# Optimization experiments

Measured on AMD Instinct MI355X. Metric: run time of the kernel, lower is better.

## Reference

```python
import jax, jax.numpy as jnp
import numpy as np

B, S, IN_DIM, EMBED, HEADS, WINDOW = 2, 2048, 1024, 1024, 16, 256
HEAD_DIM = EMBED // HEADS
NEG_FILL = -9.0e15


def setup_inputs() -> dict:
    key = jax.random.key(0)
    k1, k2, k3, k4 = jax.random.split(key, 4)
    x = jax.random.normal(k1, (B, S, IN_DIM), dtype=jnp.float32)
    # padding_mask: positions with value 1 get zeroed in q/k/v (matches masked_fill semantics)
    padding_mask = jax.random.randint(k2, (B, S), 0, 2, dtype=jnp.int32)
    # xavier-uniform-like init scale for the linear weights
    lim_qkv = np.sqrt(6.0 / (IN_DIM + 3 * EMBED)).astype(np.float32)
    lim_o = np.sqrt(6.0 / (EMBED + EMBED)).astype(np.float32)
    Wqkv = jax.random.uniform(k3, (3 * EMBED, IN_DIM), jnp.float32, -lim_qkv, lim_qkv)
    bqkv = jnp.zeros((3 * EMBED,), jnp.float32)
    Wo = jax.random.uniform(k4, (EMBED, EMBED), jnp.float32, -lim_o, lim_o)
    bo = jnp.zeros((EMBED,), jnp.float32)
    return {"x": x, "padding_mask": padding_mask, "Wqkv": Wqkv, "bqkv": bqkv, "Wo": Wo, "bo": bo}


def reference(x, padding_mask, Wqkv, bqkv, Wo, bo):
    b, s, _ = x.shape
    h, hd, pad = HEADS, HEAD_DIM, WINDOW // 2
    # qkv projection: torch Linear is x @ W.T + b
    qkv = x @ Wqkv.T + bqkv                      # [B, S, 3E]
    qkv = qkv.reshape(b, s, h, 3 * hd).transpose(0, 2, 1, 3)  # [B, H, S, 3*hd]
    q, k, v = jnp.split(qkv, 3, axis=-1)          # each [B, H, S, hd]
    # zero out padded positions in q, k, v where padding_mask == 1
    pm = (padding_mask != 0)[:, None, :, None]    # [B, 1, S, 1]
    q = jnp.where(pm, 0.0, q)
    k = jnp.where(pm, 0.0, k)
    v = jnp.where(pm, 0.0, v)
    # dense banded scores: identical math to the unfold-based band compute
    scores = jnp.einsum("bhsd,bhtd->bhst", q, k)  # [B, H, S, S]
    idx = jnp.arange(s)
    band = jnp.abs(idx[None, :] - idx[:, None]) <= pad  # |i-j| <= window/2
    scores = jnp.where(band, scores, jnp.float32(NEG_FILL))
    scores = scores / jnp.sqrt(jnp.float32(hd))   # original scales AFTER the fill
    attn = jax.nn.softmax(scores, axis=-1)        # [B, H, S, S]
    vals = jnp.einsum("bhst,bhtd->bhsd", attn, v)  # [B, H, S, hd]
    vals = vals.transpose(0, 2, 1, 3).reshape(b, s, h * hd)  # [B, S, E]
    return vals @ Wo.T + bo
```

## Files before the change

kernel.cpp:

```cpp
#include <hip/hip_runtime.h>
#include <stdint.h>

#define S_LEN 2048
#define EMBED 1024
#define HEADS 16
#define HD 64
#define M_ROWS 4096
#define N_QKV 3072
#define KDIM 1024
#define SP 2336
#define CLP2 200

typedef __attribute__((ext_vector_type(8))) short short8;
typedef __attribute__((ext_vector_type(4))) float f32x4;

__device__ __forceinline__ unsigned short f2bf(float f) {
  union { float f; uint32_t u; } c; c.f = f;
  uint32_t u = c.u;
  u += 0x7fffu + ((u >> 16) & 1u);
  return (unsigned short)(u >> 16);
}

__device__ __forceinline__ void gload_lds16(const unsigned short* g, unsigned short* l) {
  __builtin_amdgcn_global_load_lds(
      (const __attribute__((address_space(1))) void*)g,
      (__attribute__((address_space(3))) void*)l, 16, 0, 0);
}

#define XQ 1048576
#define WQKVQ 786432
#define WOQ 262144
#define CVTQ (XQ + WQKVQ + WOQ)
__global__ __launch_bounds__(256) void cvt3_kernel(
    const float* __restrict__ x, const float* __restrict__ wqkv, const float* __restrict__ wo,
    unsigned short* __restrict__ xb, unsigned short* __restrict__ wqkvb, unsigned short* __restrict__ wob,
    unsigned short* __restrict__ vTp) {
  int i = blockIdx.x * blockDim.x + threadIdx.x;
  if (i < CVTQ) {
    const float* s; unsigned short* d; int off;
    if (i < XQ)               { s = x;    d = xb;    off = i; }
    else if (i < XQ + WQKVQ)  { s = wqkv; d = wqkvb; off = i - XQ; }
    else                      { s = wo;   d = wob;   off = i - XQ - WQKVQ; }
    float4 f = reinterpret_cast<const float4*>(s)[off];
    ushort4 o;
    o.x = f2bf(f.x); o.y = f2bf(f.y); o.z = f2bf(f.z); o.w = f2bf(f.w);
    reinterpret_cast<ushort4*>(d)[off] = o;
  } else {
    int j = i - CVTQ;
    int row = j / 72, p = j % 72;
    int off = row * 584 + (p < 32 ? p : 544 + (p - 32));
    reinterpret_cast<ushort4*>(vTp)[off] = (ushort4){0, 0, 0, 0};
  }
}

__global__ __launch_bounds__(512, 2) void gemm_qkv(
    const unsigned short* __restrict__ A, const unsigned short* __restrict__ Bm,
    const float* __restrict__ bias, const int* __restrict__ pm,
    unsigned short* __restrict__ qo, unsigned short* __restrict__ ko,
    unsigned short* __restrict__ vTp)
{
  __shared__ __align__(16) unsigned short smem[57344];
  const int t = threadIdx.x, wave = t >> 6, lane = t & 63;
  const int m16 = lane & 15, q4 = lane >> 4;
  const int wm = wave >> 1, wn = wave & 1;
  const int bid = blockIdx.x;
  const int mb = bid >> 4, nb = bid & 15;
  const int lrow = lane >> 3;
  const int lsegsw = ((lane & 7) ^ lrow) * 8;
  const unsigned short* gsrc[7];
#pragma unroll
  for (int j = 0; j < 7; j++) {
    int u = wave * 7 + j;
    gsrc[j] = (u < 32 ? A  + (size_t)(mb * 256 + u * 8 + lrow) * KDIM
                      : Bm + (size_t)(nb * 192 + (u - 32) * 8 + lrow) * KDIM)
              + lsegsw;
  }
  const int rsw = (m16 & 7) * 8;

  f32x4 acc[4][6];
#pragma unroll
  for (int i_ = 0; i_ < 4; i_++)
#pragma unroll
    for (int j_ = 0; j_ < 6; j_++) acc[i_][j_] = (f32x4){0.f, 0.f, 0.f, 0.f};

  auto LDA = [&](short8* af, const unsigned short* As, int h) {
#pragma unroll
    for (int mt = 0; mt < 4; mt++)
      af[mt] = *reinterpret_cast<const short8*>(
          &As[(wm * 64 + mt * 16 + m16) * 64 + (((h * 4 + q4) * 8) ^ rsw)]);
  };
  auto LDB3 = [&](short8* bf, const unsigned short* Bs, int h, int n0) {
#pragma unroll
    for (int nt = 0; nt < 3; nt++)
      bf[nt] = *reinterpret_cast<const short8*>(
          &Bs[(wn * 96 + (n0 + nt) * 16 + m16) * 64 + (((h * 4 + q4) * 8) ^ rsw)]);
  };
  auto MM3 = [&](short8* af, short8* bf, int n0) {
#pragma unroll
    for (int mt = 0; mt < 4; mt++)
#pragma unroll
      for (int nt = 0; nt < 3; nt++)
        acc[mt][n0 + nt] =
            __builtin_amdgcn_mfma_f32_16x16x32_bf16(af[mt], bf[nt], acc[mt][n0 + nt], 0, 0, 0);
  };

#pragma unroll
  for (int j = 0; j < 7; j++)
    gload_lds16(gsrc[j], smem + (wave * 7 + j) * 512);
  __builtin_amdgcn_sched_barrier(0);

  for (int T = 0; T < 16; ++T) {
    const int c = T & 1;
    const unsigned short* As = smem + c * 28672;
    const unsigned short* Bs = As + 16384;
    unsigned short* nslab = smem + (c ^ 1) * 28672;
    const int nkt = (T + 1) * 64;
    const bool st = (T < 15);
    short8 af[4], bf[3];

    if (st) {
#pragma unroll
      for (int j = 0; j < 3; j++)
        gload_lds16(gsrc[j] + nkt, nslab + (wave * 7 + j) * 512);
    }
    __builtin_amdgcn_sched_barrier(0);
    if (st) asm volatile("s_waitcnt vmcnt(3)" ::: "memory");
    else    asm volatile("s_waitcnt vmcnt(0)" ::: "memory");
    __builtin_amdgcn_sched_barrier(0);
    __builtin_amdgcn_s_barrier();
    __builtin_amdgcn_sched_barrier(0);
    LDA(af, As, 0);
    LDB3(bf, Bs, 0, 0);
    asm volatile("s_waitcnt lgkmcnt(0)" ::: "memory");
    __builtin_amdgcn_sched_barrier(0);
    __builtin_amdgcn_s_setprio(1);
    MM3(af, bf, 0);
    __builtin_amdgcn_s_setprio(0);
    __builtin_amdgcn_sched_barrier(0);
    __builtin_amdgcn_s_barrier();
    __builtin_amdgcn_sched_barrier(0);

    LDB3(bf, Bs, 0, 3);
    if (st) {
#pragma unroll
      for (int j = 3; j < 5; j++)
        gload_lds16(gsrc[j] + nkt, nslab + (wave * 7 + j) * 512);
    }
    __builtin_amdgcn_sched_barrier(0);
    __builtin_amdgcn_s_barrier();
    asm volatile("s_waitcnt lgkmcnt(0)" ::: "memory");
    __builtin_amdgcn_sched_barrier(0);
    __builtin_amdgcn_s_setprio(1);
    MM3(af, bf, 3);
    __builtin_amdgcn_s_setprio(0);
    __builtin_amdgcn_sched_barrier(0);
    __builtin_amdgcn_s_barrier();
    __builtin_amdgcn_sched_barrier(0);

    LDA(af, As, 1);
    LDB3(bf, Bs, 1, 0);
    if (st) {
#pragma unroll
      for (int j = 5; j < 7; j++)
        gload_lds16(gsrc[j] + nkt, nslab + (wave * 7 + j) * 512);
    }
    __builtin_amdgcn_sched_barrier(0);
    __builtin_amdgcn_s_barrier();
    asm volatile("s_waitcnt lgkmcnt(0)" ::: "memory");
    __builtin_amdgcn_sched_barrier(0);
    __builtin_amdgcn_s_setprio(1);
    MM3(af, bf, 0);
    __builtin_amdgcn_s_setprio(0);
    __builtin_amdgcn_sched_barrier(0);
    __builtin_amdgcn_s_barrier();
    __builtin_amdgcn_sched_barrier(0);

    LDB3(bf, Bs, 1, 3);
    __builtin_amdgcn_sched_barrier(0);
    __builtin_amdgcn_s_barrier();
    asm volatile("s_waitcnt lgkmcnt(0)" ::: "memory");
    __builtin_amdgcn_sched_barrier(0);
    __builtin_amdgcn_s_setprio(1);
    MM3(af, bf, 3);
    __builtin_amdgcn_s_setprio(0);
    __builtin_amdgcn_sched_barrier(0);
    __builtin_amdgcn_s_barrier();
    __builtin_amdgcn_sched_barrier(0);
  }

  float pmv[4][4];
#pragma unroll
  for (int mt = 0; mt < 4; mt++)
#pragma unroll
    for (int reg = 0; reg < 4; reg++) {
      int row = mb * 256 + wm * 64 + mt * 16 + q4 * 4 + reg;
      pmv[mt][reg] = (pm[row] != 0) ? 0.0f : 1.0f;
    }
#pragma unroll
  for (int nt = 0; nt < 6; nt++) {
    int cloc = wn * 96 + nt * 16 + m16;
    float bv = bias[nb * 192 + cloc];
#pragma unroll
    for (int mt = 0; mt < 4; mt++) {
#pragma unroll
      for (int reg = 0; reg < 4; reg++) {
        int rloc = wm * 64 + mt * 16 + q4 * 4 + reg;
        smem[rloc * CLP2 + cloc] = f2bf((acc[mt][nt][reg] + bv) * pmv[mt][reg]);
      }
    }
  }
  __syncthreads();
  const int s0 = mb * 256;
  const int bh = (s0 >> 11) * 16 + nb, s0l = s0 & 2047;
  {
    int r = t >> 1, half = t & 1;
    const unsigned short* sq = &smem[r * CLP2 + half * 32];
    unsigned short* dq = qo + ((size_t)(bh * 2048 + s0l + r)) * 64 + half * 32;
#pragma unroll
    for (int j = 0; j < 4; j++)
      *reinterpret_cast<short8*>(dq + j * 8) = *reinterpret_cast<const short8*>(sq + j * 8);
    const unsigned short* sk = &smem[r * CLP2 + 64 + half * 32];
    unsigned short* dk = ko + ((size_t)(bh * 2048 + s0l + r)) * 64 + half * 32;
#pragma unroll
    for (int j = 0; j < 4; j++)
      *reinterpret_cast<short8*>(dk + j * 8) = *reinterpret_cast<const short8*>(sk + j * 8);
  }
  {
    int d = t & 63, oct = t >> 6;
    unsigned short* dst = vTp + (size_t)(bh * 64 + d) * SP + 128 + s0l + oct * 32;
#pragma unroll
    for (int j8 = 0; j8 < 4; j8++) {
      short8 tmp;
#pragma unroll
      for (int jj = 0; jj < 8; jj++)
        tmp[jj] = (short)smem[(oct * 32 + j8 * 8 + jj) * CLP2 + 128 + d];
      *reinterpret_cast<short8*>(dst + j8 * 8) = tmp;
    }
  }
}

__global__ __launch_bounds__(256) void gemm_out(
    const unsigned short* __restrict__ A, const unsigned short* __restrict__ Bm,
    const float* __restrict__ bias, float* __restrict__ out)
{
  __shared__ __align__(16) unsigned char smemraw[49152];
  float* Cldf = (float*)smemraw;
  const int t = threadIdx.x, wave = t >> 6, lane = t & 63;
  const int m16 = lane & 15, q4 = lane >> 4;
  const int wm = wave >> 1, wn = wave & 1;
  const int flat = blockIdx.y * 8 + blockIdx.x;
  const int xcd = flat & 7, bi = flat >> 3;
  const int mb = xcd * 8 + (bi & 7);
  const int nb = bi >> 3;
  const int srow = lane >> 2, scol = (lane & 3) << 3;
  const unsigned short* pA  = A + (size_t)(mb * 64 + wave * 16 + srow) * KDIM + scol;
  const unsigned short* pB0 = Bm + (size_t)(nb * 128 + wave * 32 + srow) * KDIM + scol;
  const unsigned short* pB1 = pB0 + 16 * KDIM;
  f32x4 acc[2][4];
#pragma unroll
  for (int i_ = 0; i_ < 2; i_++)
#pragma unroll
    for (int j_ = 0; j_ < 4; j_++) acc[i_][j_] = (f32x4){0.f, 0.f, 0.f, 0.f};

  auto stage = [&](int buf, int kt) {
    unsigned short* As = (unsigned short*)smemraw + buf * 12288;
    unsigned short* Bs = As + 4096;
#pragma unroll
    for (int h = 0; h < 2; h++) {
      gload_lds16(pA + kt + h * 32,  As + h * 2048 + (wave * 16) * 32);
      gload_lds16(pB0 + kt + h * 32, Bs + h * 4096 + (wave * 32) * 32);
      gload_lds16(pB1 + kt + h * 32, Bs + h * 4096 + (wave * 32 + 16) * 32);
    }
  };

  stage(0, 0);
  __builtin_amdgcn_sched_barrier(0);
  int cur = 0;
  for (int kt = 0; kt < KDIM; kt += 64) {
    const bool st = (kt + 64 < KDIM);
    if (st) stage(cur ^ 1, kt + 64);
    __builtin_amdgcn_sched_barrier(0);
    if (st) asm volatile("s_waitcnt vmcnt(6)" ::: "memory");
    else    asm volatile("s_waitcnt vmcnt(0)" ::: "memory");
    __builtin_amdgcn_sched_barrier(0);
    __builtin_amdgcn_s_barrier();
    __builtin_amdgcn_sched_barrier(0);
    const unsigned short* As = (const unsigned short*)smemraw + cur * 12288;
    const unsigned short* Bs = As + 4096;
#pragma unroll
    for (int h = 0; h < 2; h++) {
      short8 af[2], bf[4];
#pragma unroll
      for (int mt = 0; mt < 2; mt++)
        af[mt] = *reinterpret_cast<const short8*>(&As[h * 2048 + (wm * 32 + mt * 16 + m16) * 32 + q4 * 8]);
#pragma unroll
      for (int nt = 0; nt < 4; nt++)
        bf[nt] = *reinterpret_cast<const short8*>(&Bs[h * 4096 + (wn * 64 + nt * 16 + m16) * 32 + q4 * 8]);
#pragma unroll
      for (int mt = 0; mt < 2; mt++)
#pragma unroll
        for (int nt = 0; nt < 4; nt++)
          acc[mt][nt] = __builtin_amdgcn_mfma_f32_16x16x32_bf16(af[mt], bf[nt], acc[mt][nt], 0, 0, 0);
    }
    __builtin_amdgcn_sched_barrier(0);
    __builtin_amdgcn_s_barrier();
    __builtin_amdgcn_sched_barrier(0);
    cur ^= 1;
  }

#pragma unroll
  for (int nt = 0; nt < 4; nt++) {
    int cloc = wn * 64 + nt * 16 + m16;
    float bv = bias[nb * 128 + cloc];
#pragma unroll
    for (int mt = 0; mt < 2; mt++) {
#pragma unroll
      for (int reg = 0; reg < 4; reg++) {
        int rloc = wm * 32 + mt * 16 + q4 * 4 + reg;
        Cldf[rloc * 132 + cloc] = acc[mt][nt][reg] + bv;
      }
    }
  }
  __syncthreads();
  {
    int r = t >> 2, seg = t & 3;
    float* dst = out + (size_t)(mb * 64 + r) * EMBED + nb * 128 + seg * 32;
    const float* srcl = &Cldf[r * 132 + seg * 32];
#pragma unroll
    for (int j = 0; j < 8; j++)
      *reinterpret_cast<float4*>(dst + j * 4) = *reinterpret_cast<const float4*>(srcl + j * 4);
  }
}

__global__ __launch_bounds__(256, 2) void attn_kernel(
    const unsigned short* __restrict__ q, const unsigned short* __restrict__ k,
    const unsigned short* __restrict__ vTp, unsigned short* __restrict__ vals)
{
  __shared__ __align__(16) unsigned short smem[40960];
  unsigned short* Ks = smem;
  unsigned short* Vs = smem + 20480;
  unsigned short* Pld = smem;

  const int bid = blockIdx.x;
  const int bh = bid & 31, qg = bid >> 5;
  const int lane = threadIdx.x & 63, wave = threadIdx.x >> 6;
  const int i0b = qg * 64;
  const int i0 = i0b + wave * 16;
  const int m16 = lane & 15, q4 = lane >> 4;

  const unsigned short* qb = q + ((size_t)(bh * 2048 + i0 + m16)) * 64 + q4 * 8;
  short8 aq0 = *reinterpret_cast<const short8*>(qb);
  short8 aq1 = *reinterpret_cast<const short8*>(qb + 32);
  __builtin_amdgcn_sched_barrier(0);

  const unsigned short* kbase = k + (size_t)bh * 2048 * 64;
#pragma unroll
  for (int n = 0; n < 10; n++) {
    int idx = (n * 4 + wave) * 64 + lane;
    int krow = idx >> 3, seg = idx & 7;
    int grow = i0b - 128 + krow;
    grow = grow < 0 ? 0 : (grow > 2047 ? 2047 : grow);
    int lseg = seg ^ (krow & 7);
    gload_lds16(kbase + (size_t)grow * 64 + lseg * 8, Ks + (n * 4 + wave) * 512);
  }
  __builtin_amdgcn_sched_barrier(0);
  const unsigned short* vbase = vTp + (size_t)bh * 64 * SP + i0b;
#pragma unroll
  for (int n = 0; n < 10; n++) {
    int idx = (n * 4 + wave) * 64 + lane;
    int vrow = idx / 40, rem = idx % 40;
    int l = (rem & ~7) | ((rem & 7) ^ (vrow & 7));
    gload_lds16(vbase + (size_t)vrow * SP + l * 8, Vs + (n * 4 + wave) * 512);
  }
  __builtin_amdgcn_sched_barrier(0);

  asm volatile("s_waitcnt vmcnt(10)" ::: "memory");
  __builtin_amdgcn_sched_barrier(0);
  __builtin_amdgcn_s_barrier();
  __builtin_amdgcn_sched_barrier(0);

  float sum[4] = {0.f, 0.f, 0.f, 0.f};
  uint32_t pP[18][2];
#pragma unroll
  for (int ct = 0; ct < 18; ct++) {
    int r = (wave + ct) * 16 + m16;
    int js = i0b - 128 + r;
    const unsigned short* kr = Ks + r * 64;
    short8 b0 = *reinterpret_cast<const short8*>(kr + ((q4 ^ (r & 7)) * 8));
    short8 b1 = *reinterpret_cast<const short8*>(kr + (((q4 + 4) ^ (r & 7)) * 8));
    f32x4 a = {0.f, 0.f, 0.f, 0.f};
    a = __builtin_amdgcn_mfma_f32_16x16x32_bf16(aq0, b0, a, 0, 0, 0);
    a = __builtin_amdgcn_mfma_f32_16x16x32_bf16(aq1, b1, a, 0, 0, 0);
    unsigned short pe[4];
#pragma unroll
    for (int reg = 0; reg < 4; reg++) {
      int i = i0 + q4 * 4 + reg;
      bool valid = (js >= 0) && (js < 2048) && (js >= i - 128) && (js <= i + 128);
      float e = valid ? __expf(a[reg] * 0.125f) : 0.0f;
      sum[reg] += e;
      pe[reg] = f2bf(e);
    }
    pP[ct][0] = (uint32_t)pe[0] | ((uint32_t)pe[1] << 16);
    pP[ct][1] = (uint32_t)pe[2] | ((uint32_t)pe[3] << 16);
  }
  float rden[4];
#pragma unroll
  for (int reg = 0; reg < 4; reg++) {
    float s = sum[reg];
    s += __shfl_xor(s, 1);
    s += __shfl_xor(s, 2);
    s += __shfl_xor(s, 4);
    s += __shfl_xor(s, 8);
    rden[reg] = 1.0f / s;
  }

  __syncthreads();

  unsigned short* Pw = Pld + wave * 16 * 296;
#pragma unroll
  for (int ct = 0; ct < 18; ct++) {
    Pw[(q4 * 4 + 0) * 296 + ct * 16 + m16] = (unsigned short)(pP[ct][0] & 0xFFFF);
    Pw[(q4 * 4 + 1) * 296 + ct * 16 + m16] = (unsigned short)(pP[ct][0] >> 16);
    Pw[(q4 * 4 + 2) * 296 + ct * 16 + m16] = (unsigned short)(pP[ct][1] & 0xFFFF);
    Pw[(q4 * 4 + 3) * 296 + ct * 16 + m16] = (unsigned short)(pP[ct][1] >> 16);
  }
  short8 ap[9];
#pragma unroll
  for (int kc = 0; kc < 9; kc++)
    ap[kc] = *reinterpret_cast<const short8*>(&Pw[m16 * 296 + kc * 32 + q4 * 8]);

  const int b = bh >> 4, h = bh & 15;
#pragma unroll
  for (int dt = 0; dt < 4; dt++) {
    int vrow = dt * 16 + m16;
    const unsigned short* vr = Vs + vrow * 320;
    f32x4 av = {0.f, 0.f, 0.f, 0.f};
#pragma unroll
    for (int kc = 0; kc < 9; kc++) {
      int jseg = kc * 4 + wave * 2 + q4;
      if (jseg > 39) jseg = 39;
      int sseg = (jseg & ~7) | ((jseg & 7) ^ (vrow & 7));
      short8 bv = *reinterpret_cast<const short8*>(vr + sseg * 8);
      av = __builtin_amdgcn_mfma_f32_16x16x32_bf16(ap[kc], bv, av, 0, 0, 0);
    }
#pragma unroll
    for (int reg = 0; reg < 4; reg++)
      Pw[(q4 * 4 + reg) * 296 + dt * 16 + m16] = f2bf(av[reg] * rden[reg]);
  }
  {
    int srow = lane >> 2, seg = lane & 3;
    unsigned short* dst = vals + ((size_t)(b * 2048 + i0 + srow)) * 1024 + h * 64 + seg * 16;
    const unsigned short* srcl = &Pw[srow * 296 + seg * 16];
    *reinterpret_cast<short8*>(dst)     = *reinterpret_cast<const short8*>(srcl);
    *reinterpret_cast<short8*>(dst + 8) = *reinterpret_cast<const short8*>(srcl + 8);
  }
}

extern "C" void kernel_launch(void* const* d_in, const int* in_sizes, int n_in,
                              void* d_out, int out_size, void* d_ws, size_t ws_size,
                              hipStream_t stream) {
  const float* x    = (const float*)d_in[0];
  const int*   pm   = (const int*)d_in[1];
  const float* Wqkv = (const float*)d_in[2];
  const float* bqkv = (const float*)d_in[3];
  const float* Wo   = (const float*)d_in[4];
  const float* bo   = (const float*)d_in[5];
  float* out = (float*)d_out;
  char* ws = (char*)d_ws;

  unsigned short* xb    = (unsigned short*)(ws);
  unsigned short* vals  = (unsigned short*)(ws);
  unsigned short* Wqkvb = (unsigned short*)(ws +  8388608);
  unsigned short* Wob   = (unsigned short*)(ws + 14680064);
  unsigned short* qbuf  = (unsigned short*)(ws + 16777216);
  unsigned short* kbuf  = (unsigned short*)(ws + 25165824);
  unsigned short* vTp   = (unsigned short*)(ws + 33554432);

  cvt3_kernel<<<8768, 256, 0, stream>>>(x, Wqkv, Wo, xb, Wqkvb, Wob, vTp);
  gemm_qkv<<<256, 512, 0, stream>>>(xb, Wqkvb, bqkv, pm, qbuf, kbuf, vTp);
  attn_kernel<<<1024, 256, 0, stream>>>(qbuf, kbuf, vTp, vals);
  gemm_out<<<dim3(8, 64), 256, 0, stream>>>(vals, Wob, bo, out);
}
```

Baseline: 159.6 us.

## Enlarge output GEMM tile to 128x128 with swizzled LDS layout

The output projection GEMM tile grows from 64x128 to 128x128 per block, giving each wave a 64x64 sub-tile and more data reuse. The grid drops from 512 to 256 blocks. LDS staging now stores 64-wide K slabs with an XOR swizzle to avoid bank conflicts, and the MFMA bursts run at raised wave priority. In exchange the block uses more LDS and registers, and the XCD-aware block remap is dropped, which may reduce L2 locality and occupancy.

After: 159.3 us, median of 3. Within noise of the previous version (-0.1%).

```diff
diff --git a/kernel.cpp b/kernel.cpp
--- a/kernel.cpp
+++ b/kernel.cpp
@@ -243,69 +243,82 @@
     const unsigned short* __restrict__ A, const unsigned short* __restrict__ Bm,
     const float* __restrict__ bias, float* __restrict__ out)
 {
-  __shared__ __align__(16) unsigned char smemraw[49152];
+  __shared__ __align__(16) unsigned char smemraw[67584];
+  unsigned short* smem = (unsigned short*)smemraw;
   float* Cldf = (float*)smemraw;
   const int t = threadIdx.x, wave = t >> 6, lane = t & 63;
   const int m16 = lane & 15, q4 = lane >> 4;
   const int wm = wave >> 1, wn = wave & 1;
-  const int flat = blockIdx.y * 8 + blockIdx.x;
-  const int xcd = flat & 7, bi = flat >> 3;
-  const int mb = xcd * 8 + (bi & 7);
-  const int nb = bi >> 3;
-  const int srow = lane >> 2, scol = (lane & 3) << 3;
-  const unsigned short* pA  = A + (size_t)(mb * 64 + wave * 16 + srow) * KDIM + scol;
-  const unsigned short* pB0 = Bm + (size_t)(nb * 128 + wave * 32 + srow) * KDIM + scol;
-  const unsigned short* pB1 = pB0 + 16 * KDIM;
-  f32x4 acc[2][4];
-#pragma unroll
-  for (int i_ = 0; i_ < 2; i_++)
+  const int bid = blockIdx.x;
+  const int nb = bid & 7;
+  const int mb = bid >> 3;
+  const int lrow = lane >> 3;
+  const int lsegsw = ((lane & 7) ^ lrow) * 8;
+  const unsigned short* gsrc[8];
+#pragma unroll
+  for (int j = 0; j < 8; j++) {
+    int u = wave * 8 + j;
+    gsrc[j] = (u < 16 ? A  + (size_t)(mb * 128 + u * 8 + lrow) * KDIM
+                      : Bm + (size_t)(nb * 128 + (u - 16) * 8 + lrow) * KDIM)
+              + lsegsw;
+  }
+  const int rsw = (m16 & 7) * 8;
+
+  f32x4 acc[4][4];
+#pragma unroll
+  for (int i_ = 0; i_ < 4; i_++)
 #pragma unroll
     for (int j_ = 0; j_ < 4; j_++) acc[i_][j_] = (f32x4){0.f, 0.f, 0.f, 0.f};
 
-  auto stage = [&](int buf, int kt) {
-    unsigned short* As = (unsigned short*)smemraw + buf * 12288;
-    unsigned short* Bs = As + 4096;
+#pragma unroll
+  for (int j = 0; j < 8; j++)
+    gload_lds16(gsrc[j], smem + (wave * 8 + j) * 512);
+  __builtin_amdgcn_sched_barrier(0);
+
+  for (int T = 0; T < 16; ++T) {
+    const int c = T & 1;
+    const unsigned short* As = smem + c * 16384;
+    const unsigned short* Bs = As + 8192;
+    unsigned short* nslab = smem + (c ^ 1) * 16384;
+    const int nkt = (T + 1) * 64;
+    const bool st = (T < 15);
+
+    if (st) {
+#pragma unroll
+      for (int j = 0; j < 8; j++)
+        gload_lds16(gsrc[j] + nkt, nslab + (wave * 8 + j) * 512);
+    }
+    __builtin_amdgcn_sched_barrier(0);
+    if (st) asm volatile("s_waitcnt vmcnt(8)" ::: "memory");
+    else    asm volatile("s_waitcnt vmcnt(0)" ::: "memory");
+    __builtin_amdgcn_sched_barrier(0);
+    __builtin_amdgcn_s_barrier();
+    __builtin_amdgcn_sched_barrier(0);
 #pragma unroll
     for (int h = 0; h < 2; h++) {
-      gload_lds16(pA + kt + h * 32,  As + h * 2048 + (wave * 16) * 32);
-      gload_lds16(pB0 + kt + h * 32, Bs + h * 4096 + (wave * 32) * 32);
-      gload_lds16(pB1 + kt + h * 32, Bs + h * 4096 + (wave * 32 + 16) * 32);
-    }
-  };
-
-  stage(0, 0);
-  __builtin_amdgcn_sched_barrier(0);
-  int cur = 0;
-  for (int kt = 0; kt < KDIM; kt += 64) {
-    const bool st = (kt + 64 < KDIM);
-    if (st) stage(cur ^ 1, kt + 64);
-    __builtin_amdgcn_sched_barrier(0);
-    if (st) asm volatile("s_waitcnt vmcnt(6)" ::: "memory");
-    else    asm volatile("s_waitcnt vmcnt(0)" ::: "memory");
-    __builtin_amdgcn_sched_barrier(0);
-    __builtin_amdgcn_s_barrier();
-    __builtin_amdgcn_sched_barrier(0);
-    const unsigned short* As = (const unsigned short*)smemraw + cur * 12288;
-    const unsigned short* Bs = As + 4096;
-#pragma unroll
-    for (int h = 0; h < 2; h++) {
-      short8 af[2], bf[4];
-#pragma unroll
-      for (int mt = 0; mt < 2; mt++)
-        af[mt] = *reinterpret_cast<const short8*>(&As[h * 2048 + (wm * 32 + mt * 16 + m16) * 32 + q4 * 8]);
+      short8 af[4], bf[4];
+#pragma unroll
+      for (int mt = 0; mt < 4; mt++)
+        af[mt] = *reinterpret_cast<const short8*>(
+            &As[(wm * 64 + mt * 16 + m16) * 64 + (((h * 4 + q4) * 8) ^ rsw)]);
 #pragma unroll
       for (int nt = 0; nt < 4; nt++)
-        bf[nt] = *reinterpret_cast<const short8*>(&Bs[h * 4096 + (wn * 64 + nt * 16 + m16) * 32 + q4 * 8]);
-#pragma unroll
-      for (int mt = 0; mt < 2; mt++)
+        bf[nt] = *reinterpret_cast<const short8*>(
+            &Bs[(wn * 64 + nt * 16 + m16) * 64 + (((h * 4 + q4) * 8) ^ rsw)]);
+      asm volatile("s_waitcnt lgkmcnt(0)" ::: "memory");
+      __builtin_amdgcn_sched_barrier(0);
+      __builtin_amdgcn_s_setprio(1);
+#pragma unroll
+      for (int mt = 0; mt < 4; mt++)
 #pragma unroll
         for (int nt = 0; nt < 4; nt++)
           acc[mt][nt] = __builtin_amdgcn_mfma_f32_16x16x32_bf16(af[mt], bf[nt], acc[mt][nt], 0, 0, 0);
-    }
-    __builtin_amdgcn_sched_barrier(0);
-    __builtin_amdgcn_s_barrier();
-    __builtin_amdgcn_sched_barrier(0);
-    cur ^= 1;
+      __builtin_amdgcn_s_setprio(0);
+      __builtin_amdgcn_sched_barrier(0);
+    }
+    __builtin_amdgcn_sched_barrier(0);
+    __builtin_amdgcn_s_barrier();
+    __builtin_amdgcn_sched_barrier(0);
   }
 
 #pragma unroll
@@ -313,21 +326,21 @@
     int cloc = wn * 64 + nt * 16 + m16;
     float bv = bias[nb * 128 + cloc];
 #pragma unroll
-    for (int mt = 0; mt < 2; mt++) {
+    for (int mt = 0; mt < 4; mt++) {
 #pragma unroll
       for (int reg = 0; reg < 4; reg++) {
-        int rloc = wm * 32 + mt * 16 + q4 * 4 + reg;
+        int rloc = wm * 64 + mt * 16 + q4 * 4 + reg;
         Cldf[rloc * 132 + cloc] = acc[mt][nt][reg] + bv;
       }
     }
   }
   __syncthreads();
   {
-    int r = t >> 2, seg = t & 3;
-    float* dst = out + (size_t)(mb * 64 + r) * EMBED + nb * 128 + seg * 32;
-    const float* srcl = &Cldf[r * 132 + seg * 32];
-#pragma unroll
-    for (int j = 0; j < 8; j++)
+    int r = t >> 1, half = t & 1;
+    float* dst = out + (size_t)(mb * 128 + r) * EMBED + nb * 128 + half * 64;
+    const float* srcl = &Cldf[r * 132 + half * 64];
+#pragma unroll
+    for (int j = 0; j < 16; j++)
       *reinterpret_cast<float4*>(dst + j * 4) = *reinterpret_cast<const float4*>(srcl + j * 4);
   }
 }
@@ -479,5 +492,5 @@
   cvt3_kernel<<<8768, 256, 0, stream>>>(x, Wqkv, Wo, xb, Wqkvb, Wob, vTp);
   gemm_qkv<<<256, 512, 0, stream>>>(xb, Wqkvb, bqkv, pm, qbuf, kbuf, vTp);
   attn_kernel<<<1024, 256, 0, stream>>>(qbuf, kbuf, vTp, vals);
-  gemm_out<<<dim3(8, 64), 256, 0, stream>>>(vals, Wob, bo, out);
-}
+  gemm_out<<<256, 256, 0, stream>>>(vals, Wob, bo, out);
+}
```
